# Performance work log

Hardware: AMD Instinct MI355X
Metric: run time of the kernel (lower is better)

The kernel has to match this reference:

```python
import jax, jax.numpy as jnp
import numpy as np

EPS = 0.5      # sinkhorn eps used by assign_batch_sinkhorn
NITERS = 15    # sinkhorn iterations used by assign_batch_sinkhorn


def pairwise_dists(features, centroids):
    # ||f - c|| via the expansion ||f||^2 + ||c||^2 - 2 f.c (avoids the
    # [B, nc, D] intermediate the naive broadcast would materialize).
    f2 = jnp.sum(features * features, axis=-1)          # [B]
    c2 = jnp.sum(centroids * centroids, axis=-1)        # [K]
    d2 = f2[:, None] + c2[None, :] - 2.0 * features @ centroids.T  # [B, K]
    return jnp.sqrt(jnp.maximum(d2, 0.0))


def sinkhorn(scores, eps=EPS, niters=NITERS):
    # Faithful to the torch sinkhorn(): Q = exp(scores/eps).T, normalize
    # columns (sum over K), then alternate row/column scalings.
    Q = jnp.exp(scores / eps).T                          # [K, B]
    Q = Q / jnp.sum(Q, axis=0, keepdims=True)
    K, B = Q.shape
    r = jnp.ones((K,), Q.dtype) / K
    c = jnp.ones((B,), Q.dtype) / B

    def body(_, Q):
        Q = Q * (r / jnp.sum(Q, axis=1))[:, None]
        Q = Q * (c / jnp.sum(Q, axis=0))[None, :]
        return Q

    Q = jax.lax.fori_loop(0, niters, body, Q)
    return (Q / jnp.sum(Q, axis=0, keepdims=True)).T     # [B, K]


def setup_inputs() -> dict:
    key = jax.random.key(0)
    kf, kc = jax.random.split(key)
    B, K, D = 16384, 2048, 1000
    # 0.1 scale keeps dists ~O(5) so exp(-dists/eps) stays in fp32 range
    # (unit-randn 1000-dim features give dists ~45 -> exp underflow).
    features = 0.1 * jax.random.normal(kf, (B, D), dtype=jnp.float32)
    centroids = 0.1 * jax.random.normal(kc, (K, D), dtype=jnp.float32)
    return {"features": features, "centroids": centroids}


def reference(features, centroids):
    B, K = features.shape[0], centroids.shape[0]
    dists = pairwise_dists(features, centroids)          # [B, K]

    # assign_batch_sinkhorn (soft assignments computed under no_grad)
    soft = jax.lax.stop_gradient(sinkhorn(-dists))       # [B, K]
    batch_assignments = jnp.argmin(soft, axis=1)         # [B] (as in source)
    soft_counts = jnp.sum(soft, axis=0)                  # [K]
    cluster_loss = jnp.mean(
        jnp.take_along_axis(dists, batch_assignments[:, None], axis=1))

    # the per-element python count loops, as fused scatter-adds
    cluster_counts = jnp.zeros((K,), jnp.int32).at[batch_assignments].add(1)
    raw_assign = jnp.argmin(dists, axis=1)
    raw_counts = jnp.zeros((K,), jnp.int32).at[raw_assign].add(1)

    return cluster_loss, batch_assignments, soft_counts, cluster_counts, raw_counts
```

## Files before the change

kernel.cpp:

```cpp
#include <hip/hip_runtime.h>

typedef __attribute__((ext_vector_type(8))) short bf16x8;
typedef __attribute__((ext_vector_type(8))) unsigned short ushort8_t;
typedef __attribute__((ext_vector_type(4))) float f32x4;
typedef __attribute__((ext_vector_type(16))) float f32x16;

#define NB 16384
#define NK 2048
#define ND 1000
#define KP 1024
#define NCHK 1024

__device__ ushort g_E[(size_t)NB * NK];
__device__ ushort g_R[(size_t)NB * NK];
__device__ ushort g_Fh[(size_t)NB * KP], g_Fl[(size_t)NB * KP];
__device__ ushort g_Ch[(size_t)NK * KP], g_Cl[(size_t)NK * KP];
__device__ float  g_u[NK], g_c2[NK];
__device__ float  g_f2[NB], g_bd[NB];
__device__ float  g_part[(size_t)NCHK * NK];
__device__ int    g_cc[NK], g_rc[NK];

typedef const __attribute__((address_space(1))) void gvoid_t;
typedef __attribute__((address_space(3))) void lvoid_t;

union h16 { ushort u; _Float16 h; };

__device__ __forceinline__ ushort bf16_rne(float x){
    uint u = __float_as_uint(x);
    uint lsb = (u >> 16) & 1u;
    u += 0x7fffu + lsb;
    return (ushort)(u >> 16);
}
__device__ __forceinline__ float bf16_to_f(ushort h){
    return __uint_as_float(((uint)h) << 16);
}

__global__ __launch_bounds__(256) void cn_prep(const float* __restrict__ F,
                                               const float* __restrict__ Cn){
    const int isC = (blockIdx.x >= NB);
    const int row = isC ? (blockIdx.x - NB) : blockIdx.x;
    const float* __restrict__ X = isC ? Cn : F;
    ushort* __restrict__ H = isC ? g_Ch : g_Fh;
    ushort* __restrict__ L = isC ? g_Cl : g_Fl;
    float*  __restrict__ sq = isC ? g_c2 : g_f2;
    const int t = threadIdx.x;
    const int lane = t & 63, wid = t >> 6;
    if (isC && t == 0){ g_cc[row] = 0; g_rc[row] = 0; }
    float4 x = make_float4(0.f,0.f,0.f,0.f);
    if (t < 250) x = *(const float4*)(X + (size_t)row * ND + 4 * t);
    double s = (double)x.x*x.x + (double)x.y*x.y + (double)x.z*x.z + (double)x.w*x.w;
    ushort4 h4, l4;
#pragma unroll
    for (int c = 0; c < 4; ++c){
        float xc = (&x.x)[c];
        ushort h = bf16_rne(xc);
        (&h4.x)[c] = h;
        (&l4.x)[c] = bf16_rne(xc - bf16_to_f(h));
    }
    const int base = (t >> 4) << 6;
    const int g    = (t >> 1) & 7;
    const int hp   = (g >> 2) ^ (row & 1);
    const int sub  = (g & 3) ^ ((row >> 1) & 3);
    const int pos  = base + (hp << 5) + (sub << 3) + ((t & 1) << 2);
    *(ushort4*)&H[(size_t)row * KP + pos] = h4;
    *(ushort4*)&L[(size_t)row * KP + pos] = l4;

    __shared__ double pr[4];
    for (int off = 32; off; off >>= 1) s += __shfl_xor(s, off);
    if (lane == 0) pr[wid] = s;
    __syncthreads();
    if (t == 0) sq[row] = (float)(pr[0] + pr[1] + pr[2] + pr[3]);
}

__global__ __launch_bounds__(256) void cn_gemm_dist(){
    __shared__ __attribute__((aligned(16))) ushort Ah[128 * 64];
    __shared__ __attribute__((aligned(16))) ushort Al[128 * 64];
    __shared__ __attribute__((aligned(16))) ushort Bh[128 * 64];
    __shared__ __attribute__((aligned(16))) ushort Bl[128 * 64];

    const int tid = threadIdx.x;
    const int lane = tid & 63, wid = tid >> 6;
    const int wr = wid >> 1, wc = wid & 1;
    const int brow0 = blockIdx.y * 128, bcol0 = blockIdx.x * 128;

    f32x16 acc[2][2];
#pragma unroll
    for (int mt = 0; mt < 2; ++mt)
#pragma unroll
        for (int nt = 0; nt < 2; ++nt)
#pragma unroll
            for (int r = 0; r < 16; ++r) acc[mt][nt][r] = 0.f;

    const int srow = lane >> 3;
    const int sgr  = lane & 7;

    const int arow = wr * 64 + (lane & 31);
    const int brow = wc * 64 + (lane & 31);
    const int kh   = lane >> 5;
    const int b0k  = lane & 1;
    const int b12  = (lane >> 1) & 3;

    for (int kt = 0; kt < 16; ++kt){
        const int k0 = kt * 64;
#pragma unroll
        for (int c4 = 0; c4 < 4; ++c4){
            const int ch = wid * 4 + c4;
            const int ldso = ch * 512;
            const size_t ga = (size_t)(brow0 + ch * 8 + srow) * KP + k0 + sgr * 8;
            const size_t gb = (size_t)(bcol0 + ch * 8 + srow) * KP + k0 + sgr * 8;
            __builtin_amdgcn_global_load_lds((gvoid_t*)(g_Fh + ga), (lvoid_t*)(Ah + ldso), 16, 0, 0);
            __builtin_amdgcn_global_load_lds((gvoid_t*)(g_Fl + ga), (lvoid_t*)(Al + ldso), 16, 0, 0);
            __builtin_amdgcn_global_load_lds((gvoid_t*)(g_Ch + gb), (lvoid_t*)(Bh + ldso), 16, 0, 0);
            __builtin_amdgcn_global_load_lds((gvoid_t*)(g_Cl + gb), (lvoid_t*)(Bl + ldso), 16, 0, 0);
        }
        __syncthreads();

#pragma unroll
        for (int ks = 0; ks < 4; ++ks){
            const int g  = ks * 2 + kh;
            const int off = (((g >> 2) ^ b0k) << 5) + (((g & 3) ^ b12) << 3);
            bf16x8 a_h[2], a_l[2], b_h[2], b_l[2];
#pragma unroll
            for (int mt = 0; mt < 2; ++mt){
                const int ro = (arow + mt * 32) * 64 + off;
                a_h[mt] = *(const bf16x8*)&Ah[ro];
                a_l[mt] = *(const bf16x8*)&Al[ro];
            }
#pragma unroll
            for (int nt = 0; nt < 2; ++nt){
                const int ro = (brow + nt * 32) * 64 + off;
                b_h[nt] = *(const bf16x8*)&Bh[ro];
                b_l[nt] = *(const bf16x8*)&Bl[ro];
            }
#pragma unroll
            for (int mt = 0; mt < 2; ++mt)
#pragma unroll
                for (int nt = 0; nt < 2; ++nt){
                    acc[mt][nt] = __builtin_amdgcn_mfma_f32_32x32x16_bf16(a_h[mt], b_h[nt], acc[mt][nt], 0, 0, 0);
                    acc[mt][nt] = __builtin_amdgcn_mfma_f32_32x32x16_bf16(a_h[mt], b_l[nt], acc[mt][nt], 0, 0, 0);
                    acc[mt][nt] = __builtin_amdgcn_mfma_f32_32x32x16_bf16(a_l[mt], b_h[nt], acc[mt][nt], 0, 0, 0);
                }
        }
        __syncthreads();
    }

#pragma unroll
    for (int mt = 0; mt < 2; ++mt){
#pragma unroll
        for (int nt = 0; nt < 2; ++nt){
            const int col = bcol0 + wc * 64 + nt * 32 + (lane & 31);
            const float c2v = g_c2[col];
#pragma unroll
            for (int reg = 0; reg < 16; ++reg){
                const int row = brow0 + wr * 64 + mt * 32 + (reg & 3) + 8 * (reg >> 2) + 4 * kh;
                float d2 = g_f2[row] + c2v - 2.0f * acc[mt][nt][reg];
                float d  = sqrtf(fmaxf(d2, 0.0f));
                float e32 = __expf(-2.0f * d) * 8192.0f;
                size_t idx = (size_t)row * NK + col;
                h16 hv; hv.h = (_Float16)e32;
                float hf = (float)hv.h;
                h16 rv; rv.h = (_Float16)(e32 - hf);
                g_E[idx] = hv.u;
                g_R[idx] = rv.u;
            }
        }
    }
}

template<int MODE>
__global__ __launch_bounds__(256) void cn_sweep(float* __restrict__ outba){
    __shared__ float4 sred[3][8][64];
    const int lane = threadIdx.x & 63, wid = threadIdx.x >> 6;
    const int row0 = (blockIdx.x * 4 + wid) * 4;
    const float cst = (MODE == 0) ? 1.0f : (1.0f / (float)NB);

    float4 uu[8];
    if (MODE >= 1){
#pragma unroll
        for (int j = 0; j < 4; ++j)
#pragma unroll
            for (int h = 0; h < 2; ++h)
                uu[2 * j + h] = *(const float4*)&g_u[512 * j + 8 * lane + 4 * h];
    }

    float4 S[8];
#pragma unroll
    for (int j = 0; j < 8; ++j) S[j] = make_float4(0.f,0.f,0.f,0.f);

    for (int r = 0; r < 4; ++r){
        const int b = row0 + r;
        float tsum = 0.f;
        if (MODE <= 1){
            ushort8_t q8[4];
            const ushort* er = g_E + (size_t)b * NK + 8 * lane;
#pragma unroll
            for (int j = 0; j < 4; ++j){
                q8[j] = *(const ushort8_t*)(er + 512 * j);
#pragma unroll
                for (int c = 0; c < 8; ++c){
                    h16 cv; cv.u = q8[j][c];
                    float e = (float)cv.h;
                    tsum += (MODE == 1) ? e * (&uu[2 * j + (c >> 2)].x)[c & 3] : e;
                }
            }
#pragma unroll
            for (int off = 32; off; off >>= 1) tsum += __shfl_xor(tsum, off);
            const float v = cst / tsum;
#pragma unroll
            for (int j = 0; j < 4; ++j)
#pragma unroll
                for (int c = 0; c < 8; ++c){
                    h16 cv; cv.u = q8[j][c];
                    (&S[2 * j + (c >> 2)].x)[c & 3] += (float)cv.h * v;
                }
        } else {
            float ev[4][8];
            const ushort* er = g_E + (size_t)b * NK + 8 * lane;
            const ushort* rr = g_R + (size_t)b * NK + 8 * lane;
#pragma unroll
            for (int j = 0; j < 4; ++j){
                ushort8_t qe = *(const ushort8_t*)(er + 512 * j);
                ushort8_t qr = *(const ushort8_t*)(rr + 512 * j);
#pragma unroll
                for (int c = 0; c < 8; ++c){
                    h16 cv; cv.u = qe[c];
                    h16 rv; rv.u = qr[c];
                    float e = (float)cv.h + (float)rv.h;
                    ev[j][c] = e;
                    tsum += e * (&uu[2 * j + (c >> 2)].x)[c & 3];
                }
            }
#pragma unroll
            for (int off = 32; off; off >>= 1) tsum += __shfl_xor(tsum, off);
            const float v = cst / tsum;
#pragma unroll
            for (int j = 0; j < 4; ++j)
#pragma unroll
                for (int c = 0; c < 8; ++c)
                    (&S[2 * j + (c >> 2)].x)[c & 3] += ev[j][c] * v;

            if (MODE == 3){
                double bestW = 1.0e300; int bi = 0; float be = 1.f;
                float rbe = -1.f;      int ri = 0;
#pragma unroll
                for (int j = 0; j < 4; ++j){
#pragma unroll
                    for (int c = 0; c < 8; ++c){
                        int k = 512 * j + 8 * lane + c;
                        float e = ev[j][c];
                        double w = (double)e * (double)(&uu[2 * j + (c >> 2)].x)[c & 3];
                        if (w < bestW){ bestW = w; bi = k; be = e; }
                        if (e > rbe){ rbe = e; ri = k; }
                    }
                }
                for (int off = 32; off; off >>= 1){
                    double oW = __shfl_xor(bestW, off);
                    int    oi = __shfl_xor(bi, off);
                    float  oe = __shfl_xor(be, off);
                    if (oW < bestW || (oW == bestW && oi < bi)){ bestW = oW; bi = oi; be = oe; }
                    float ore = __shfl_xor(rbe, off);
                    int   ori = __shfl_xor(ri, off);
                    if (ore > rbe || (ore == rbe && ori < ri)){ rbe = ore; ri = ori; }
                }
                if (lane == 0){
                    outba[b] = (float)bi;
                    g_bd[b] = (float)(-0.5 * (log((double)be) - 9.010913347279288));
                    atomicAdd(&g_cc[bi], 1);
                    atomicAdd(&g_rc[ri], 1);
                }
            }
        }
    }

    if (wid > 0){
#pragma unroll
        for (int j = 0; j < 8; ++j) sred[wid - 1][j][lane] = S[j];
    }
    __syncthreads();
    if (wid == 0){
#pragma unroll
        for (int w = 0; w < 3; ++w)
#pragma unroll
            for (int j = 0; j < 8; ++j){
                float4 o = sred[w][j][lane];
                S[j].x += o.x; S[j].y += o.y; S[j].z += o.z; S[j].w += o.w;
            }
#pragma unroll
        for (int j = 0; j < 4; ++j)
#pragma unroll
            for (int h = 0; h < 2; ++h)
                *(float4*)&g_part[(size_t)blockIdx.x * NK + 512 * j + 8 * lane + 4 * h] = S[2 * j + h];
    }
}

__global__ __launch_bounds__(256) void cn_red0(){
    __shared__ double red[4][8];
    const int kk  = threadIdx.x & 7;
    const int sub = threadIdx.x >> 3;
    const int wv  = threadIdx.x >> 6;
    const int k = blockIdx.x * 8 + kk;
    double s = 0.0;
#pragma unroll 8
    for (int i = 0; i < 32; ++i)
        s += (double)g_part[(size_t)(i * 32 + sub) * NK + k];
    s += __shfl_xor(s, 8); s += __shfl_xor(s, 16); s += __shfl_xor(s, 32);
    if ((threadIdx.x & 63) < 8) red[wv][kk] = s;
    __syncthreads();
    if (threadIdx.x < 8){
        double tot = red[0][kk] + red[1][kk] + red[2][kk] + red[3][kk];
        g_u[blockIdx.x * 8 + kk] = (float)((1.0 / (double)NK) / tot);
    }
}

__global__ __launch_bounds__(256) void cn_fin(float* __restrict__ out){
    __shared__ double red[4][64];
    __shared__ double lred[4];
    const int lane = threadIdx.x & 63, q = threadIdx.x >> 6;
    const int k = blockIdx.x * 64 + lane;
    double s = 0.0;
    for (int ch = q * 256; ch < q * 256 + 256; ++ch)
        s += (double)g_part[(size_t)ch * NK + k];
    red[q][lane] = s;
    __syncthreads();
    if (q == 0){
        double tot = red[0][lane] + red[1][lane] + red[2][lane] + red[3][lane];
        out[1 + NB + k] = (float)((double)NB * (double)g_u[k] * tot);
    } else if (q == 1){
        out[1 + NB + NK + k] = (float)g_cc[k];
    } else if (q == 2){
        out[1 + NB + 2 * NK + k] = (float)g_rc[k];
    }
    if (blockIdx.x == 0){
        double sl = 0.0;
        for (int b = threadIdx.x; b < NB; b += 256) sl += (double)g_bd[b];
        for (int off = 32; off; off >>= 1) sl += __shfl_xor(sl, off);
        if (lane == 0) lred[q] = sl;
        __syncthreads();
        if (threadIdx.x == 0)
            out[0] = (float)((lred[0] + lred[1] + lred[2] + lred[3]) / (double)NB);
    }
}

extern "C" void kernel_launch(void* const* d_in, const int* in_sizes, int n_in,
                              void* d_out, int out_size, void* d_ws, size_t ws_size,
                              hipStream_t stream){
    const float* F  = (const float*)d_in[0];
    const float* Cn = (const float*)d_in[1];
    float* out = (float*)d_out;
    (void)d_ws; (void)ws_size;

    cn_prep<<<NB + NK, 256, 0, stream>>>(F, Cn);

    dim3 gg(NK / 128, NB / 128);
    cn_gemm_dist<<<gg, 256, 0, stream>>>();

    cn_sweep<0><<<NCHK, 256, 0, stream>>>(nullptr);
    cn_red0<<<NK / 8, 256, 0, stream>>>();
    for (int it = 1; it <= 11; ++it){
        cn_sweep<1><<<NCHK, 256, 0, stream>>>(nullptr);
        cn_red0<<<NK / 8, 256, 0, stream>>>();
    }
    for (int it = 12; it <= 14; ++it){
        cn_sweep<2><<<NCHK, 256, 0, stream>>>(nullptr);
        cn_red0<<<NK / 8, 256, 0, stream>>>();
    }
    cn_sweep<3><<<NCHK, 256, 0, stream>>>(out + 1);
    cn_fin<<<NK / 64, 256, 0, stream>>>(out);
}
```

Before: 710.2 us.

## Fuse per-iteration column reduction into sweep via last-arriving-block atomic counter

Removes the separate cn_red0 launch after each Sinkhorn sweep. Each sweep block increments a per-iteration global counter. The last 256 blocks to arrive wait until all blocks have written their partials, then each reduces an 8-column slice and writes the scaling vector. This cuts launch overhead and inter-kernel gaps, but adds spin-waiting and depends on the arrival order for forward progress.

```diff
diff --git a/kernel.cpp b/kernel.cpp
--- a/kernel.cpp
+++ b/kernel.cpp
@@ -10,6 +10,7 @@
 #define ND 1000
 #define KP 1024
 #define NCHK 1024
+#define NRED 256
 
 __device__ ushort g_E[(size_t)NB * NK];
 __device__ ushort g_R[(size_t)NB * NK];
@@ -19,6 +20,7 @@
 __device__ float  g_f2[NB], g_bd[NB];
 __device__ float  g_part[(size_t)NCHK * NK];
 __device__ int    g_cc[NK], g_rc[NK];
+__device__ uint   g_ctr[24];
 
 typedef const __attribute__((address_space(1))) void gvoid_t;
 typedef __attribute__((address_space(3))) void lvoid_t;
@@ -46,6 +48,7 @@
     const int t = threadIdx.x;
     const int lane = t & 63, wid = t >> 6;
     if (isC && t == 0){ g_cc[row] = 0; g_rc[row] = 0; }
+    if (blockIdx.x == 0 && t < 24) g_ctr[t] = 0;
     float4 x = make_float4(0.f,0.f,0.f,0.f);
     if (t < 250) x = *(const float4*)(X + (size_t)row * ND + 4 * t);
     double s = (double)x.x*x.x + (double)x.y*x.y + (double)x.z*x.z + (double)x.w*x.w;
@@ -168,8 +171,10 @@
 }
 
 template<int MODE>
-__global__ __launch_bounds__(256) void cn_sweep(float* __restrict__ outba){
+__global__ __launch_bounds__(256) void cn_sweep(float* __restrict__ outba, int IT){
     __shared__ float4 sred[3][8][64];
+    __shared__ double redd[4][8];
+    __shared__ int sh_arr;
     const int lane = threadIdx.x & 63, wid = threadIdx.x >> 6;
     const int row0 = (blockIdx.x * 4 + wid) * 4;
     const float cst = (MODE == 0) ? 1.0f : (1.0f / (float)NB);
@@ -291,24 +296,40 @@
             for (int h = 0; h < 2; ++h)
                 *(float4*)&g_part[(size_t)blockIdx.x * NK + 512 * j + 8 * lane + 4 * h] = S[2 * j + h];
     }
-}
-
-__global__ __launch_bounds__(256) void cn_red0(){
-    __shared__ double red[4][8];
-    const int kk  = threadIdx.x & 7;
-    const int sub = threadIdx.x >> 3;
-    const int wv  = threadIdx.x >> 6;
-    const int k = blockIdx.x * 8 + kk;
-    double s = 0.0;
+
+    if (MODE <= 2){
+        __syncthreads();
+        if (threadIdx.x == 0){
+            __threadfence();
+            sh_arr = (int)__hip_atomic_fetch_add(&g_ctr[IT], 1u, __ATOMIC_ACQ_REL, __HIP_MEMORY_SCOPE_AGENT);
+        }
+        __syncthreads();
+        const int arr = sh_arr;
+        if (arr >= NCHK - NRED){
+            if (threadIdx.x == 0){
+                while (__hip_atomic_load(&g_ctr[IT], __ATOMIC_ACQUIRE, __HIP_MEMORY_SCOPE_AGENT) < NCHK)
+                    __builtin_amdgcn_s_sleep(4);
+                __threadfence();
+            }
+            __syncthreads();
+            const int slice = arr - (NCHK - NRED);
+            const int kk  = threadIdx.x & 7;
+            const int sub = threadIdx.x >> 3;
+            const int wv  = threadIdx.x >> 6;
+            const int k = slice * 8 + kk;
+            double s = 0.0;
 #pragma unroll 8
-    for (int i = 0; i < 32; ++i)
-        s += (double)g_part[(size_t)(i * 32 + sub) * NK + k];
-    s += __shfl_xor(s, 8); s += __shfl_xor(s, 16); s += __shfl_xor(s, 32);
-    if ((threadIdx.x & 63) < 8) red[wv][kk] = s;
-    __syncthreads();
-    if (threadIdx.x < 8){
-        double tot = red[0][kk] + red[1][kk] + red[2][kk] + red[3][kk];
-        g_u[blockIdx.x * 8 + kk] = (float)((1.0 / (double)NK) / tot);
+            for (int i = 0; i < 32; ++i)
+                s += (double)g_part[(size_t)(i * 32 + sub) * NK + k];
+            s += __shfl_xor(s, 8); s += __shfl_xor(s, 16); s += __shfl_xor(s, 32);
+            if ((threadIdx.x & 63) < 8) redd[wv][kk] = s;
+            __syncthreads();
+            if (threadIdx.x < 8){
+                double tot = redd[0][threadIdx.x] + redd[1][threadIdx.x] +
+                             redd[2][threadIdx.x] + redd[3][threadIdx.x];
+                g_u[slice * 8 + threadIdx.x] = (float)((1.0 / (double)NK) / tot);
+            }
+        }
     }
 }
 
@@ -354,16 +375,11 @@
     dim3 gg(NK / 128, NB / 128);
     cn_gemm_dist<<<gg, 256, 0, stream>>>();
 
-    cn_sweep<0><<<NCHK, 256, 0, stream>>>(nullptr);
-    cn_red0<<<NK / 8, 256, 0, stream>>>();
-    for (int it = 1; it <= 11; ++it){
-        cn_sweep<1><<<NCHK, 256, 0, stream>>>(nullptr);
-        cn_red0<<<NK / 8, 256, 0, stream>>>();
-    }
-    for (int it = 12; it <= 14; ++it){
-        cn_sweep<2><<<NCHK, 256, 0, stream>>>(nullptr);
-        cn_red0<<<NK / 8, 256, 0, stream>>>();
-    }
-    cn_sweep<3><<<NCHK, 256, 0, stream>>>(out + 1);
+    cn_sweep<0><<<NCHK, 256, 0, stream>>>(nullptr, 0);
+    for (int it = 1; it <= 11; ++it)
+        cn_sweep<1><<<NCHK, 256, 0, stream>>>(nullptr, it);
+    for (int it = 12; it <= 14; ++it)
+        cn_sweep<2><<<NCHK, 256, 0, stream>>>(nullptr, it);
+    cn_sweep<3><<<NCHK, 256, 0, stream>>>(out + 1, 15);
     cn_fin<<<NK / 64, 256, 0, stream>>>(out);
 }
```

New measurement: 2.098 ms. 2.95x slower.
